# Performance work log

Measured on AMD Instinct MI355X. Metric: run time of the kernel, lower is better.

The kernel has to match this reference:

```python
import jax, jax.numpy as jnp
import numpy as np

# Full panorama / crop constants hardcoded in the original cal_offset
H_FULL, W_FULL = 438, 1285
CROP_H, CROP_W = 384, 384
FV_ORI, FH_ORI = 123.5, 360.0  # vertical / horizontal FOV in degrees
CHUNK = 512


def transform(x, sh, sw):
    """Spherical depth image -> XYZ point cloud. x: [b,1,h,w].
    Faithful to the original: only the LAST batch element survives the loop."""
    d = x[-1, 0]  # [h, w]
    h, w = d.shape
    crop_w_rad = sw / W_FULL * FH_ORI  # degrees despite the name (as in source)
    crop_h_rad = sh / H_FULL * FV_ORI
    fv_crop = FV_ORI * CROP_H / H_FULL
    fh_crop = FH_ORI * CROP_W / W_FULL
    rows = jnp.arange(h, dtype=d.dtype)
    cols = jnp.arange(w, dtype=d.dtype)
    yaw = jnp.deg2rad(-fh_crop * cols / w + crop_w_rad)    # [w]
    pitch = jnp.deg2rad(-fv_crop * rows / h + crop_h_rad)  # [h]
    sin_p = jnp.sin(pitch)[:, None]
    cos_p = jnp.cos(pitch)[:, None]
    X = d * jnp.sin(yaw)[None, :] * sin_p
    Y = d * jnp.cos(yaw)[None, :] * sin_p
    Z = d * cos_p
    return jnp.stack([X, Y, Z], axis=-1).reshape(-1, 3)  # [h*w, 3]


def _nn_indices(A, B):
    """For each point in A [N,3], index of nearest point in B [M,3] (sq. dist).
    Chunked over A so the distance block is [CHUNK, M], never [N, M]."""
    B_sq = jnp.sum(B * B, axis=-1)  # [M]
    n = A.shape[0]
    A_ch = A.reshape(n // CHUNK, CHUNK, 3)

    def one_chunk(a):  # a: [CHUNK, 3]
        d = jnp.sum(a * a, axis=-1)[:, None] + B_sq[None, :] - 2.0 * (a @ B.T)
        return jnp.argmin(d, axis=-1)  # [CHUNK]

    return jax.lax.map(one_chunk, A_ch).reshape(-1)  # [N]


def chamfer(P, Q):
    """Symmetric Chamfer: mean min squared distance both directions."""
    i_pq = jax.lax.stop_gradient(_nn_indices(P, Q))
    i_qp = jax.lax.stop_gradient(_nn_indices(Q, P))
    dist1 = jnp.sum((P - Q[i_pq]) ** 2, axis=-1)  # [N]
    dist2 = jnp.sum((Q - P[i_qp]) ** 2, axis=-1)  # [M]
    return jnp.mean(dist1) + jnp.mean(dist2)


def setup_inputs() -> dict:
    key = jax.random.key(0)
    k1, k2 = jax.random.split(key)
    # depths in a realistic LiDAR range (positive)
    fake = jax.random.uniform(k1, (1, 1, 384, 384), dtype=jnp.float32) * 50.0
    tar = jax.random.uniform(k2, (1, 1, 384, 384), dtype=jnp.float32) * 50.0
    return {"fake": fake, "tar": tar, "sh": 27, "sw": 100}


def reference(fake, tar, sh, sw):
    points = transform(tar, sh, sw)                # [N, 3]
    points_reconstructed = transform(fake, sh, sw)  # [N, 3]
    return chamfer(points, points_reconstructed)
```

## Files before the change

### kernel.cpp

```cpp
#include <hip/hip_runtime.h>
#include <math.h>


#define N_PTS 147456
#define N2    (2 * N_PTS)
#define IMG_W 384
#define G     48
#define NC    (G * G * G)
#define NCI   (2 * NC)
#define SCALE 0.48f
#define HC    2.0833333f
#define SCAN_BLOCKS 864


__device__ __forceinline__ float4 transform_pt(
    int idx, const float* __restrict__ fake, const float* __restrict__ tar,
    int sh, int sw)
{
    int pix = (idx < N_PTS) ? idx : idx - N_PTS;
    int r = pix / IMG_W, c = pix - r * IMG_W;
    float cw = (float)((double)sw / 1285.0 * 360.0);
    float ch = (float)((double)sh / 438.0 * 123.5);
    const float fh = (float)(360.0 * 384.0 / 1285.0);
    const float fv = (float)(123.5 * 384.0 / 438.0);
    const float D2R = 0.017453292519943295f;
    float yaw = ((-fh * (float)c) / 384.0f + cw) * D2R;
    float pit = ((-fv * (float)r) / 384.0f + ch) * D2R;
    float sy = sinf(yaw), cy = cosf(yaw);
    float sp = sinf(pit), cp = cosf(pit);
    float d = (idx < N_PTS) ? tar[pix] : fake[pix];
    return make_float4(d * sy * sp, d * cy * sp, d * cp, 0.f);
}

__device__ __forceinline__ int cell_coord(float v) {
    int c = (int)((v + 50.0f) * SCALE);
    return min(max(c, 0), G - 1);
}

__device__ __forceinline__ int cell_of(float x, float y, float z) {
    return (cell_coord(z) * G + cell_coord(y)) * G + cell_coord(x);
}


__global__ __launch_bounds__(256) void zero_kernel(int* __restrict__ p) {
    p[blockIdx.x * 256 + threadIdx.x] = 0;
}

__global__ __launch_bounds__(256) void count_kernel(
    const float* __restrict__ fake, const float* __restrict__ tar,
    const int* __restrict__ sh_p, const int* __restrict__ sw_p,
    int* __restrict__ offc)
{
    int idx = blockIdx.x * 256 + threadIdx.x;
    float4 p = transform_pt(idx, fake, tar, *sh_p, *sw_p);
    int bucket = ((idx < N_PTS) ? 0 : NC) + cell_of(p.x, p.y, p.z);
    atomicAdd(&offc[bucket], 1);
}

__global__ __launch_bounds__(256) void scan1_kernel(
    int* __restrict__ offc, int* __restrict__ bsum)
{
    __shared__ int sd[256];
    int t = threadIdx.x;
    int gid = blockIdx.x * 256 + t;
    int c = offc[gid];
    sd[t] = c;
    __syncthreads();
    for (int o = 1; o < 256; o <<= 1) {
        int v = (t >= o) ? sd[t - o] : 0;
        __syncthreads();
        sd[t] += v;
        __syncthreads();
    }
    offc[gid] = sd[t] - c;
    if (t == 255) bsum[blockIdx.x] = sd[255];
}

__global__ __launch_bounds__(1024) void scan2_kernel(int* __restrict__ bsum)
{
    __shared__ int sd[1024];
    int t = threadIdx.x;
    int v0 = (t < SCAN_BLOCKS) ? bsum[t] : 0;
    sd[t] = v0;
    __syncthreads();
    for (int o = 1; o < 1024; o <<= 1) {
        int v = (t >= o) ? sd[t - o] : 0;
        __syncthreads();
        sd[t] += v;
        __syncthreads();
    }
    if (t < SCAN_BLOCKS) bsum[t] = sd[t] - v0;
}

__global__ __launch_bounds__(256) void scan3_kernel(
    int* __restrict__ offc, const int* __restrict__ bsum)
{
    int gid = blockIdx.x * 256 + threadIdx.x;
    offc[gid] += bsum[blockIdx.x];
}

__global__ __launch_bounds__(256) void fill_kernel(
    const float* __restrict__ fake, const float* __restrict__ tar,
    const int* __restrict__ sh_p, const int* __restrict__ sw_p,
    int* __restrict__ offc, float4* __restrict__ pts)
{
    int idx = blockIdx.x * 256 + threadIdx.x;
    float4 p = transform_pt(idx, fake, tar, *sh_p, *sw_p);
    int bucket = ((idx < N_PTS) ? 0 : NC) + cell_of(p.x, p.y, p.z);
    int slot = atomicAdd(&offc[bucket], 1);
    pts[slot] = make_float4(p.x, p.y, p.z, 0.f);
}

#define SCAN_RANGE(LO, HI)                                                  \
    for (int j = (LO) + lane; j < (HI); j += 64) {                          \
        float4 t = pts[j];                                                  \
        float ddx = t.x - qx, ddy = t.y - qy, ddz = t.z - qz;               \
        best = fminf(best, fmaf(ddx, ddx, fmaf(ddy, ddy, ddz * ddz)));      \
    }

#define WAVE_MIN(B)                                                         \
    _Pragma("unroll")                                                       \
    for (int o = 32; o; o >>= 1) (B) = fminf((B), __shfl_xor((B), o, 64));

__global__ __launch_bounds__(256) void query_kernel(
    float4* __restrict__ pts, const int* __restrict__ offc)
{
    const int lane = threadIdx.x & 63;
    const int g = blockIdx.x * 4 + (threadIdx.x >> 6);
    float4 q = pts[g];
    const float qx = q.x, qy = q.y, qz = q.z;
    const int base = __builtin_amdgcn_readfirstlane((g < N_PTS) ? NC : 0);

    const int cx = __builtin_amdgcn_readfirstlane(cell_coord(qx));
    const int cy = __builtin_amdgcn_readfirstlane(cell_coord(qy));
    const int cz = __builtin_amdgcn_readfirstlane(cell_coord(qz));
    float fx = (qx + 50.0f) * SCALE - (float)cx;
    float fy = (qy + 50.0f) * SCALE - (float)cy;
    float fz = (qz + 50.0f) * SCALE - (float)cz;
    float m = fmaxf(fminf(fminf(fminf(fx, 1.0f - fx), fminf(fy, 1.0f - fy)),
                          fminf(fz, 1.0f - fz)), 0.0f);

    float best = __builtin_inff();

    {
        int c0 = base + (cz * G + cy) * G + cx;
        int lo = c0 ? offc[c0 - 1] : 0;
        int hi = offc[c0];
        SCAN_RANGE(lo, hi)
    }
    WAVE_MIN(best)
    float m2 = m * HC;
    if (best > m2 * m2) {
        const float HC2 = HC * HC;
        float bestU = best;
        #pragma unroll
        for (int dz = -1; dz <= 1; dz++) {
            int iz = cz + dz;
            if (iz < 0 || iz >= G) continue;
            float dzl = (dz == 0) ? 0.f : ((dz > 0) ? (1.f - fz) : fz);
            #pragma unroll
            for (int dy = -1; dy <= 1; dy++) {
                int iy = cy + dy;
                if (iy < 0 || iy >= G) continue;
                int rowb = base + (iz * G + iy) * G;
                if (dz == 0 && dy == 0) {
                    if (cx - 1 >= 0 && fx * fx * HC2 < bestU) {
                        int c0 = rowb + cx - 1;
                        int lo = c0 ? offc[c0 - 1] : 0;
                        int hi = offc[c0];
                        SCAN_RANGE(lo, hi)
                    }
                    if (cx + 1 < G && (1.f - fx) * (1.f - fx) * HC2 < bestU) {
                        int c0 = rowb + cx + 1;
                        int lo = c0 ? offc[c0 - 1] : 0;
                        int hi = offc[c0];
                        SCAN_RANGE(lo, hi)
                    }
                } else {
                    float dyl = (dy == 0) ? 0.f : ((dy > 0) ? (1.f - fy) : fy);
                    if ((dzl * dzl + dyl * dyl) * HC2 < bestU) {
                        int c0 = rowb + max(cx - 1, 0);
                        int c1 = rowb + min(cx + 1, G - 1);
                        int lo = c0 ? offc[c0 - 1] : 0;
                        int hi = offc[c1];
                        SCAN_RANGE(lo, hi)
                    }
                }
            }
        }
        WAVE_MIN(best)
        float bnd1 = (1.0f + m) * HC;
        if (best > bnd1 * bnd1) {
            for (int s = 2; s <= G; ++s) {
                int zlo = max(cz - s, 0), zhi = min(cz + s, G - 1);
                for (int iz = zlo; iz <= zhi; ++iz) {
                    int adz = iz - cz; adz = (adz < 0) ? -adz : adz;
                    int ylo = max(cy - s, 0), yhi = min(cy + s, G - 1);
                    for (int iy = ylo; iy <= yhi; ++iy) {
                        int ady = iy - cy; ady = (ady < 0) ? -ady : ady;
                        int rowb = base + (iz * G + iy) * G;
                        if (adz == s || ady == s) {
                            int c0 = rowb + max(cx - s, 0);
                            int c1 = rowb + min(cx + s, G - 1);
                            int lo = c0 ? offc[c0 - 1] : 0;
                            int hi = offc[c1];
                            SCAN_RANGE(lo, hi)
                        } else {
                            if (cx - s >= 0) {
                                int c0 = rowb + cx - s;
                                int lo = c0 ? offc[c0 - 1] : 0;
                                int hi = offc[c0];
                                SCAN_RANGE(lo, hi)
                            }
                            if (cx + s <= G - 1) {
                                int c0 = rowb + cx + s;
                                int lo = c0 ? offc[c0 - 1] : 0;
                                int hi = offc[c0];
                                SCAN_RANGE(lo, hi)
                            }
                        }
                    }
                }
                WAVE_MIN(best)
                float bnd = ((float)s + m) * HC;
                if (best <= bnd * bnd) break;
            }
        }
    }

    if (lane == 0) pts[g].w = best;
}

__global__ __launch_bounds__(256) void reduce1(
    const float4* __restrict__ pts, float* __restrict__ partials)
{
    int tid = threadIdx.x;
    int basei = blockIdx.x * 1024;
    float s = 0.f;
    #pragma unroll
    for (int t = 0; t < 4; t++) s += pts[basei + t * 256 + tid].w;
    #pragma unroll
    for (int o = 32; o; o >>= 1) s += __shfl_xor(s, o, 64);
    __shared__ float wsum[4];
    if ((tid & 63) == 0) wsum[tid >> 6] = s;
    __syncthreads();
    if (tid == 0) partials[blockIdx.x] = wsum[0] + wsum[1] + wsum[2] + wsum[3];
}

__global__ __launch_bounds__(256) void reduce2(
    const float* __restrict__ partials, float* __restrict__ out)
{
    int tid = threadIdx.x;
    float s = 0.f;
    for (int i = tid; i < 288; i += 256) s += partials[i];
    #pragma unroll
    for (int o = 32; o; o >>= 1) s += __shfl_xor(s, o, 64);
    __shared__ float wsum[4];
    if ((tid & 63) == 0) wsum[tid >> 6] = s;
    __syncthreads();
    if (tid == 0) out[0] = (wsum[0] + wsum[1] + wsum[2] + wsum[3]) / 147456.0f;
}

extern "C" void kernel_launch(void* const* d_in, const int* in_sizes, int n_in,
                              void* d_out, int out_size, void* d_ws, size_t ws_size,
                              hipStream_t stream) {
    const float* fake = (const float*)d_in[0];
    const float* tar  = (const float*)d_in[1];
    const int*   sh_p = (const int*)d_in[2];
    const int*   sw_p = (const int*)d_in[3];
    float* out = (float*)d_out;

    int* wsi = (int*)d_ws;
    int*    offc  = wsi;
    int*    bsum  = wsi + NCI;
    float*  parts = (float*)(wsi + NCI + 1024);
    float4* pts   = (float4*)(wsi + NCI + 1312);

    zero_kernel<<<SCAN_BLOCKS, 256, 0, stream>>>(offc);
    count_kernel<<<N2 / 256, 256, 0, stream>>>(fake, tar, sh_p, sw_p, offc);
    scan1_kernel<<<SCAN_BLOCKS, 256, 0, stream>>>(offc, bsum);
    scan2_kernel<<<1, 1024, 0, stream>>>(bsum);
    scan3_kernel<<<SCAN_BLOCKS, 256, 0, stream>>>(offc, bsum);
    fill_kernel<<<N2 / 256, 256, 0, stream>>>(fake, tar, sh_p, sw_p, offc, pts);
    query_kernel<<<N2 / 4, 256, 0, stream>>>(pts, offc);
    reduce1<<<N2 / 1024, 256, 0, stream>>>(pts, parts);
    reduce2<<<1, 256, 0, stream>>>(parts, out);
}
```

Before: 455.2 us.

## Fuse grid build stages into one cooperative kernel and merge final reductions

Replaces the zero, count, three-pass scan and fill kernels with a single cooperative kernel that separates the phases with grid-wide syncs. Each of the 864 blocks handles both its own point and an extra point offset by NCI, and block 0 does the scan of block sums. The two reduction kernels become one, using an atomic counter so the last block does the final sum. The aim is to cut kernel launch overhead and inter-kernel gaps, at the cost of grid-sync latency and a cooperative launch that needs all blocks resident at once.

```diff
diff --git a/kernel.cpp b/kernel.cpp
--- a/kernel.cpp
+++ b/kernel.cpp
@@ -1,6 +1,9 @@
 #include <hip/hip_runtime.h>
+#include <hip/hip_cooperative_groups.h>
 #include <math.h>
 
+
+namespace cg = cooperative_groups;
 
 #define N_PTS 147456
 #define N2    (2 * N_PTS)
@@ -10,7 +13,7 @@
 #define NCI   (2 * NC)
 #define SCALE 0.48f
 #define HC    2.0833333f
-#define SCAN_BLOCKS 864
+#define BUILD_BLOCKS 864
 
 
 __device__ __forceinline__ float4 transform_pt(
@@ -41,75 +44,81 @@
     return (cell_coord(z) * G + cell_coord(y)) * G + cell_coord(x);
 }
 
-
-__global__ __launch_bounds__(256) void zero_kernel(int* __restrict__ p) {
-    p[blockIdx.x * 256 + threadIdx.x] = 0;
-}
-
-__global__ __launch_bounds__(256) void count_kernel(
+__global__ __launch_bounds__(256, 4) void build_kernel(
     const float* __restrict__ fake, const float* __restrict__ tar,
     const int* __restrict__ sh_p, const int* __restrict__ sw_p,
-    int* __restrict__ offc)
+    int* __restrict__ offc, int* __restrict__ bsum, int* __restrict__ counter,
+    float4* __restrict__ pts)
 {
-    int idx = blockIdx.x * 256 + threadIdx.x;
-    float4 p = transform_pt(idx, fake, tar, *sh_p, *sw_p);
-    int bucket = ((idx < N_PTS) ? 0 : NC) + cell_of(p.x, p.y, p.z);
-    atomicAdd(&offc[bucket], 1);
-}
-
-__global__ __launch_bounds__(256) void scan1_kernel(
-    int* __restrict__ offc, int* __restrict__ bsum)
-{
+    cg::grid_group grid = cg::this_grid();
+    const int tid = threadIdx.x;
+    const int bid = blockIdx.x;
+    const int gid = bid * 256 + tid;
+
+    offc[gid] = 0;
+    if (bid == 0) {
+        #pragma unroll
+        for (int i = 0; i < 4; i++) bsum[tid + i * 256] = 0;
+        if (tid == 0) *counter = 0;
+    }
+    grid.sync();
+
+    const int sh = *sh_p, sw = *sw_p;
+    float4 p0 = transform_pt(gid, fake, tar, sh, sw);
+    int b0 = ((gid < N_PTS) ? 0 : NC) + cell_of(p0.x, p0.y, p0.z);
+    atomicAdd(&offc[b0], 1);
+    const int gid1 = gid + NCI;
+    float4 p1; int b1 = -1;
+    if (gid1 < N2) {
+        p1 = transform_pt(gid1, fake, tar, sh, sw);
+        b1 = NC + cell_of(p1.x, p1.y, p1.z);
+        atomicAdd(&offc[b1], 1);
+    }
+    grid.sync();
+
     __shared__ int sd[256];
-    int t = threadIdx.x;
-    int gid = blockIdx.x * 256 + t;
     int c = offc[gid];
-    sd[t] = c;
+    sd[tid] = c;
     __syncthreads();
     for (int o = 1; o < 256; o <<= 1) {
-        int v = (t >= o) ? sd[t - o] : 0;
+        int v = (tid >= o) ? sd[tid - o] : 0;
         __syncthreads();
-        sd[t] += v;
+        sd[tid] += v;
         __syncthreads();
     }
-    offc[gid] = sd[t] - c;
-    if (t == 255) bsum[blockIdx.x] = sd[255];
-}
-
-__global__ __launch_bounds__(1024) void scan2_kernel(int* __restrict__ bsum)
-{
-    __shared__ int sd[1024];
-    int t = threadIdx.x;
-    int v0 = (t < SCAN_BLOCKS) ? bsum[t] : 0;
-    sd[t] = v0;
-    __syncthreads();
-    for (int o = 1; o < 1024; o <<= 1) {
-        int v = (t >= o) ? sd[t - o] : 0;
+    offc[gid] = sd[tid] - c;
+    if (tid == 255) bsum[bid] = sd[255];
+    grid.sync();
+
+    if (bid == 0) {
+        int b4[4]; int s = 0;
+        #pragma unroll
+        for (int i = 0; i < 4; i++) { b4[i] = bsum[tid * 4 + i]; s += b4[i]; }
+        sd[tid] = s;
         __syncthreads();
-        sd[t] += v;
-        __syncthreads();
-    }
-    if (t < SCAN_BLOCKS) bsum[t] = sd[t] - v0;
-}
-
-__global__ __launch_bounds__(256) void scan3_kernel(
-    int* __restrict__ offc, const int* __restrict__ bsum)
-{
-    int gid = blockIdx.x * 256 + threadIdx.x;
-    offc[gid] += bsum[blockIdx.x];
-}
-
-__global__ __launch_bounds__(256) void fill_kernel(
-    const float* __restrict__ fake, const float* __restrict__ tar,
-    const int* __restrict__ sh_p, const int* __restrict__ sw_p,
-    int* __restrict__ offc, float4* __restrict__ pts)
-{
-    int idx = blockIdx.x * 256 + threadIdx.x;
-    float4 p = transform_pt(idx, fake, tar, *sh_p, *sw_p);
-    int bucket = ((idx < N_PTS) ? 0 : NC) + cell_of(p.x, p.y, p.z);
-    int slot = atomicAdd(&offc[bucket], 1);
-    pts[slot] = make_float4(p.x, p.y, p.z, 0.f);
-}
+        for (int o = 1; o < 256; o <<= 1) {
+            int v = (tid >= o) ? sd[tid - o] : 0;
+            __syncthreads();
+            sd[tid] += v;
+            __syncthreads();
+        }
+        int run = sd[tid] - s;
+        #pragma unroll
+        for (int i = 0; i < 4; i++) { int cc = b4[i]; bsum[tid * 4 + i] = run; run += cc; }
+    }
+    grid.sync();
+
+    offc[gid] += bsum[bid];
+    grid.sync();
+
+    int slot0 = atomicAdd(&offc[b0], 1);
+    pts[slot0] = make_float4(p0.x, p0.y, p0.z, 0.f);
+    if (b1 >= 0) {
+        int slot1 = atomicAdd(&offc[b1], 1);
+        pts[slot1] = make_float4(p1.x, p1.y, p1.z, 0.f);
+    }
+}
+
 
 #define SCAN_RANGE(LO, HI)                                                  \
     for (int j = (LO) + lane; j < (HI); j += 64) {                          \
@@ -231,34 +240,39 @@
     if (lane == 0) pts[g].w = best;
 }
 
-__global__ __launch_bounds__(256) void reduce1(
-    const float4* __restrict__ pts, float* __restrict__ partials)
+__global__ __launch_bounds__(256) void reduce_kernel(
+    const float4* __restrict__ pts, float* __restrict__ partials,
+    int* __restrict__ counter, float* __restrict__ out)
 {
-    int tid = threadIdx.x;
-    int basei = blockIdx.x * 1024;
+    const int tid = threadIdx.x;
+    const int basei = blockIdx.x * 1024;
     float s = 0.f;
     #pragma unroll
     for (int t = 0; t < 4; t++) s += pts[basei + t * 256 + tid].w;
     #pragma unroll
     for (int o = 32; o; o >>= 1) s += __shfl_xor(s, o, 64);
     __shared__ float wsum[4];
+    __shared__ int lastflag;
     if ((tid & 63) == 0) wsum[tid >> 6] = s;
     __syncthreads();
-    if (tid == 0) partials[blockIdx.x] = wsum[0] + wsum[1] + wsum[2] + wsum[3];
-}
-
-__global__ __launch_bounds__(256) void reduce2(
-    const float* __restrict__ partials, float* __restrict__ out)
-{
-    int tid = threadIdx.x;
-    float s = 0.f;
-    for (int i = tid; i < 288; i += 256) s += partials[i];
-    #pragma unroll
-    for (int o = 32; o; o >>= 1) s += __shfl_xor(s, o, 64);
-    __shared__ float wsum[4];
-    if ((tid & 63) == 0) wsum[tid >> 6] = s;
+    if (tid == 0) {
+        partials[blockIdx.x] = wsum[0] + wsum[1] + wsum[2] + wsum[3];
+        __threadfence();
+        int old = atomicAdd(counter, 1);
+        lastflag = (old == 287);
+    }
     __syncthreads();
-    if (tid == 0) out[0] = (wsum[0] + wsum[1] + wsum[2] + wsum[3]) / 147456.0f;
+    if (lastflag) {
+        __threadfence();
+        float s2 = 0.f;
+        for (int i = tid; i < 288; i += 256) s2 += partials[i];
+        #pragma unroll
+        for (int o = 32; o; o >>= 1) s2 += __shfl_xor(s2, o, 64);
+        if ((tid & 63) == 0) wsum[tid >> 6] = s2;
+        __syncthreads();
+        if (tid == 0)
+            out[0] = (wsum[0] + wsum[1] + wsum[2] + wsum[3]) / 147456.0f;
+    }
 }
 
 extern "C" void kernel_launch(void* const* d_in, const int* in_sizes, int n_in,
@@ -271,18 +285,16 @@
     float* out = (float*)d_out;
 
     int* wsi = (int*)d_ws;
-    int*    offc  = wsi;
-    int*    bsum  = wsi + NCI;
-    float*  parts = (float*)(wsi + NCI + 1024);
-    float4* pts   = (float4*)(wsi + NCI + 1312);
-
-    zero_kernel<<<SCAN_BLOCKS, 256, 0, stream>>>(offc);
-    count_kernel<<<N2 / 256, 256, 0, stream>>>(fake, tar, sh_p, sw_p, offc);
-    scan1_kernel<<<SCAN_BLOCKS, 256, 0, stream>>>(offc, bsum);
-    scan2_kernel<<<1, 1024, 0, stream>>>(bsum);
-    scan3_kernel<<<SCAN_BLOCKS, 256, 0, stream>>>(offc, bsum);
-    fill_kernel<<<N2 / 256, 256, 0, stream>>>(fake, tar, sh_p, sw_p, offc, pts);
+    int*    offc    = wsi;
+    int*    bsum    = wsi + NCI;
+    int*    counter = wsi + NCI + 1024;
+    float*  parts   = (float*)(wsi + NCI + 1056);
+    float4* pts     = (float4*)(wsi + NCI + 1344);
+
+    void* args[] = { (void*)&fake, (void*)&tar, (void*)&sh_p, (void*)&sw_p,
+                     (void*)&offc, (void*)&bsum, (void*)&counter, (void*)&pts };
+    hipLaunchCooperativeKernel((const void*)build_kernel,
+                               dim3(BUILD_BLOCKS), dim3(256), args, 0, stream);
     query_kernel<<<N2 / 4, 256, 0, stream>>>(pts, offc);
-    reduce1<<<N2 / 1024, 256, 0, stream>>>(pts, parts);
-    reduce2<<<1, 256, 0, stream>>>(parts, out);
-}
+    reduce_kernel<<<N2 / 1024, 256, 0, stream>>>(pts, parts, counter, out);
+}
```

Measured after the change: 831.1 us. +82.6%, slower.

## Replace three-pass scan with decoupled look-back and fuse final reduction

Applied to the files above, without the earlier changes.

The three scan kernels become a single-pass scan. Each block publishes its aggregate and inclusive prefix through flag words, and a wave walks back through predecessor flags to build its prefix. The two reduction kernels are merged into one that uses an atomic counter so the last block finishes the final sum. This cuts three kernel launches and their serialization gaps, in exchange for spin-waiting on predecessor flags and relying on the order in which blocks are scheduled.

```diff
diff --git a/kernel.cpp b/kernel.cpp
--- a/kernel.cpp
+++ b/kernel.cpp
@@ -11,6 +11,8 @@
 #define SCALE 0.48f
 #define HC    2.0833333f
 #define SCAN_BLOCKS 864
+#define ZERO_BLOCKS 868
+#define VAL_MASK 0x3FFFFFFF
 
 
 __device__ __forceinline__ float4 transform_pt(
@@ -57,12 +59,13 @@
     atomicAdd(&offc[bucket], 1);
 }
 
-__global__ __launch_bounds__(256) void scan1_kernel(
-    int* __restrict__ offc, int* __restrict__ bsum)
+__global__ __launch_bounds__(256) void scan_kernel(
+    int* __restrict__ offc, int* __restrict__ flag)
 {
     __shared__ int sd[256];
-    int t = threadIdx.x;
-    int gid = blockIdx.x * 256 + t;
+    __shared__ int pfx_s;
+    const int t = threadIdx.x, b = blockIdx.x;
+    const int gid = b * 256 + t;
     int c = offc[gid];
     sd[t] = c;
     __syncthreads();
@@ -72,31 +75,44 @@
         sd[t] += v;
         __syncthreads();
     }
-    offc[gid] = sd[t] - c;
-    if (t == 255) bsum[blockIdx.x] = sd[255];
-}
-
-__global__ __launch_bounds__(1024) void scan2_kernel(int* __restrict__ bsum)
-{
-    __shared__ int sd[1024];
-    int t = threadIdx.x;
-    int v0 = (t < SCAN_BLOCKS) ? bsum[t] : 0;
-    sd[t] = v0;
+    const int incl = sd[t];
+    const int agg = sd[255];
+    if (t == 0) {
+        unsigned w = ((b == 0 ? 2u : 1u) << 30) | (unsigned)agg;
+        __hip_atomic_store(&flag[b], (int)w, __ATOMIC_RELEASE, __HIP_MEMORY_SCOPE_AGENT);
+    }
+    if (t < 64) {
+        const int lane = t;
+        int prefix = 0;
+        if (b > 0) {
+            int iw = b - 1 - lane;
+            bool done = false;
+            while (!done) {
+                int w = (iw >= 0)
+                    ? __hip_atomic_load(&flag[iw], __ATOMIC_ACQUIRE, __HIP_MEMORY_SCOPE_AGENT)
+                    : (int)(2u << 30);
+                unsigned st = ((unsigned)w) >> 30;
+                unsigned long long m2 = __ballot(st == 2u);
+                unsigned long long m0 = __ballot(st == 0u);
+                int f2 = m2 ? (__ffsll((unsigned long long)m2) - 1) : 64;
+                int f0 = m0 ? (__ffsll((unsigned long long)m0) - 1) : 64;
+                if (f0 < f2) { __builtin_amdgcn_s_sleep(1); continue; }
+                int val = (lane <= f2) ? (w & VAL_MASK) : 0;
+                #pragma unroll
+                for (int o = 32; o; o >>= 1) val += __shfl_xor(val, o, 64);
+                prefix += val;
+                if (f2 < 64) done = true;
+                else iw -= 64;
+            }
+            if (lane == 0) {
+                unsigned w2 = (2u << 30) | (unsigned)(prefix + agg);
+                __hip_atomic_store(&flag[b], (int)w2, __ATOMIC_RELEASE, __HIP_MEMORY_SCOPE_AGENT);
+            }
+        }
+        if (lane == 0) pfx_s = prefix;
+    }
     __syncthreads();
-    for (int o = 1; o < 1024; o <<= 1) {
-        int v = (t >= o) ? sd[t - o] : 0;
-        __syncthreads();
-        sd[t] += v;
-        __syncthreads();
-    }
-    if (t < SCAN_BLOCKS) bsum[t] = sd[t] - v0;
-}
-
-__global__ __launch_bounds__(256) void scan3_kernel(
-    int* __restrict__ offc, const int* __restrict__ bsum)
-{
-    int gid = blockIdx.x * 256 + threadIdx.x;
-    offc[gid] += bsum[blockIdx.x];
+    offc[gid] = pfx_s + incl - c;
 }
 
 __global__ __launch_bounds__(256) void fill_kernel(
@@ -110,6 +126,7 @@
     int slot = atomicAdd(&offc[bucket], 1);
     pts[slot] = make_float4(p.x, p.y, p.z, 0.f);
 }
+
 
 #define SCAN_RANGE(LO, HI)                                                  \
     for (int j = (LO) + lane; j < (HI); j += 64) {                          \
@@ -231,34 +248,39 @@
     if (lane == 0) pts[g].w = best;
 }
 
-__global__ __launch_bounds__(256) void reduce1(
-    const float4* __restrict__ pts, float* __restrict__ partials)
-{
-    int tid = threadIdx.x;
-    int basei = blockIdx.x * 1024;
+__global__ __launch_bounds__(256) void reduce_kernel(
+    const float4* __restrict__ pts, float* __restrict__ partials,
+    int* __restrict__ counter, float* __restrict__ out)
+{
+    const int tid = threadIdx.x;
+    const int basei = blockIdx.x * 1024;
     float s = 0.f;
     #pragma unroll
     for (int t = 0; t < 4; t++) s += pts[basei + t * 256 + tid].w;
     #pragma unroll
     for (int o = 32; o; o >>= 1) s += __shfl_xor(s, o, 64);
     __shared__ float wsum[4];
+    __shared__ int lastflag;
     if ((tid & 63) == 0) wsum[tid >> 6] = s;
     __syncthreads();
-    if (tid == 0) partials[blockIdx.x] = wsum[0] + wsum[1] + wsum[2] + wsum[3];
-}
-
-__global__ __launch_bounds__(256) void reduce2(
-    const float* __restrict__ partials, float* __restrict__ out)
-{
-    int tid = threadIdx.x;
-    float s = 0.f;
-    for (int i = tid; i < 288; i += 256) s += partials[i];
-    #pragma unroll
-    for (int o = 32; o; o >>= 1) s += __shfl_xor(s, o, 64);
-    __shared__ float wsum[4];
-    if ((tid & 63) == 0) wsum[tid >> 6] = s;
+    if (tid == 0) {
+        partials[blockIdx.x] = wsum[0] + wsum[1] + wsum[2] + wsum[3];
+        __threadfence();
+        int old = atomicAdd(counter, 1);
+        lastflag = (old == 287);
+    }
     __syncthreads();
-    if (tid == 0) out[0] = (wsum[0] + wsum[1] + wsum[2] + wsum[3]) / 147456.0f;
+    if (lastflag) {
+        __threadfence();
+        float s2 = 0.f;
+        for (int i = tid; i < 288; i += 256) s2 += partials[i];
+        #pragma unroll
+        for (int o = 32; o; o >>= 1) s2 += __shfl_xor(s2, o, 64);
+        if ((tid & 63) == 0) wsum[tid >> 6] = s2;
+        __syncthreads();
+        if (tid == 0)
+            out[0] = (wsum[0] + wsum[1] + wsum[2] + wsum[3]) / 147456.0f;
+    }
 }
 
 extern "C" void kernel_launch(void* const* d_in, const int* in_sizes, int n_in,
@@ -271,18 +293,16 @@
     float* out = (float*)d_out;
 
     int* wsi = (int*)d_ws;
-    int*    offc  = wsi;
-    int*    bsum  = wsi + NCI;
-    float*  parts = (float*)(wsi + NCI + 1024);
-    float4* pts   = (float4*)(wsi + NCI + 1312);
-
-    zero_kernel<<<SCAN_BLOCKS, 256, 0, stream>>>(offc);
+    int*    offc    = wsi;
+    int*    flags   = wsi + NCI;
+    int*    counter = wsi + NCI + 864;
+    float*  parts   = (float*)(wsi + NCI + 1024);
+    float4* pts     = (float4*)(wsi + NCI + 1312);
+
+    zero_kernel<<<ZERO_BLOCKS, 256, 0, stream>>>(wsi);
     count_kernel<<<N2 / 256, 256, 0, stream>>>(fake, tar, sh_p, sw_p, offc);
-    scan1_kernel<<<SCAN_BLOCKS, 256, 0, stream>>>(offc, bsum);
-    scan2_kernel<<<1, 1024, 0, stream>>>(bsum);
-    scan3_kernel<<<SCAN_BLOCKS, 256, 0, stream>>>(offc, bsum);
+    scan_kernel<<<SCAN_BLOCKS, 256, 0, stream>>>(offc, flags);
     fill_kernel<<<N2 / 256, 256, 0, stream>>>(fake, tar, sh_p, sw_p, offc, pts);
     query_kernel<<<N2 / 4, 256, 0, stream>>>(pts, offc);
-    reduce1<<<N2 / 1024, 256, 0, stream>>>(pts, parts);
-    reduce2<<<1, 256, 0, stream>>>(parts, out);
-}
+    reduce_kernel<<<N2 / 1024, 256, 0, stream>>>(pts, parts, counter, out);
+}
```

New measurement: 504.6 us. +10.9%, slower.
